# Performance work log

Hardware: AMD Instinct MI355X
Metric: run time of the kernel (lower is better)

## Reference

```python
import jax, jax.numpy as jnp
import numpy as np


def setup_inputs() -> dict:
    key = jax.random.key(0)
    k1, k2 = jax.random.split(key)
    x = jax.random.normal(k1, (16, 128, 64, 64), dtype=jnp.float32)
    # weight layout: [out_channels, in_channels, kh, kw], kernel must be 3 for the
    # original Python-loop bounds to match the allocated output size
    weight = jax.random.normal(k2, (256, 128, 3, 3), dtype=jnp.float32) * 0.05
    return {"x": x, "weight": weight}


def reference(x, weight):
    # Stride-1 conv2d with symmetric zero padding=1 (forward ignores bias/stride/
    # dilation/groups in the original module).
    pad = 1
    out = jax.lax.conv_general_dilated(
        x, weight,
        window_strides=(1, 1),
        padding=[(pad, pad), (pad, pad)],
        dimension_numbers=("NCHW", "OIHW", "NCHW"),
    )
    return out
```

## Files before the change

kernel.cpp:

```cpp
#include <hip/hip_runtime.h>
#include <hip/hip_bf16.h>
#include <stdint.h>

typedef short bf16x8 __attribute__((ext_vector_type(8)));
typedef float f32x16 __attribute__((ext_vector_type(16)));

#define N_IMG 16
#define C_IN  128
#define H_IMG 64
#define W_IMG 64
#define K_OUT 256

#define XB_BYTES (16ull*66*66*128*2)
#define WB_BYTES (36ull*8*2*64*16)
#define WS_NEED  (XB_BYTES + WB_BYTES)

#define LDSX_BYTES (6*66*256)

__device__ __forceinline__ void gload16(void* lds, const void* g) {
    __builtin_amdgcn_global_load_lds(
        (const __attribute__((address_space(1))) void*)g,
        (__attribute__((address_space(3))) void*)lds, 16, 0, 0);
}

__device__ __forceinline__ uint32_t pack2(float a, float b) {
    __hip_bfloat16 ha = __float2bfloat16(a), hb = __float2bfloat16(b);
    return (uint32_t)*(uint16_t*)&ha | ((uint32_t)*(uint16_t*)&hb << 16);
}

__global__ __launch_bounds__(256)
void transform_fused_kernel(const float* __restrict__ x, const float* __restrict__ w,
                            __hip_bfloat16* __restrict__ xb, __hip_bfloat16* __restrict__ wb) {
    __shared__ __align__(16) uint32_t xs[64 * 64];
    __shared__ float lw[1152];
    const int b = blockIdx.x;
    const int t = threadIdx.x;

    if (b < 1056) {
        const int yt = b % 66;
        const int n  = b / 66;
        const bool interior = (yt >= 1 && yt <= 64);

        if (interior) {
            const float4* src = (const float4*)(x + (size_t)n * 524288 + (size_t)(yt - 1) * 64);
            #pragma unroll
            for (int it = 0; it < 4; ++it) {
                const int x4 = t & 15;
                const int j  = (t >> 4) + it * 16;
                float4 va = src[(2 * j) * 1024 + x4];
                float4 vb = src[(2 * j + 1) * 1024 + x4];
                const float* pa = (const float*)&va;
                const float* pb = (const float*)&vb;
                #pragma unroll
                for (int i = 0; i < 4; ++i) {
                    int row = x4 * 4 + i;
                    xs[row * 64 + (j ^ (((row >> 2) & 3) << 2))] = pack2(pa[i], pb[i]);
                }
            }
        }
        __syncthreads();

        uint4* dst = (uint4*)((char*)xb + (size_t)(n * 66 + yt) * 66 * 256);
        #pragma unroll
        for (int it = 0; it < 5; ++it) {
            int ch = t + it * 256;
            if (ch < 1056) {
                int xt = ch >> 4, u = ch & 15;
                uint4 val = make_uint4(0u, 0u, 0u, 0u);
                if (interior && xt >= 1 && xt <= 64) {
                    int row = xt - 1;
                    val = *(const uint4*)&xs[row * 64 + 4 * (u ^ ((row >> 2) & 3))];
                }
                dst[ch] = val;
            }
        }
    } else {
        const int kg = b - 1056;
        for (int e = t; e < 1152; e += 256) lw[e] = w[kg * 1152 + e];
        __syncthreads();
        const int basek = (kg >> 5) * 1024 + (kg & 31) * 8;
        #pragma unroll
        for (int tap = 0; tap < 9; ++tap) {
            if (t < 128) {
                int c = t;
                int idx = (tap * 4 + (c >> 5)) * 8192 + basek
                        + ((c >> 4) & 1) * 512 + ((c >> 3) & 1) * 256 + (c & 7);
                wb[idx] = __float2bfloat16(lw[c * 9 + tap]);
            }
        }
    }
}

#define CHUNK(CC, AU, XBN)                                                                    \
  {                                                                                           \
    _Pragma("unroll") for (int f = 0; f < 4; ++f)                         \
      x1[f] = *(const bf16x8*)(lds + (xb0[f] ^ (((CC) << 6) | 32)));                          \
    __builtin_amdgcn_s_setprio(1);                                                            \
    _Pragma("unroll") for (int f = 0; f < 4; ++f) {                                           \
      acc[0][f] = __builtin_amdgcn_mfma_f32_32x32x16_bf16(AU[0][0], x0[f], acc[0][f], 0, 0, 0); \
      acc[1][f] = __builtin_amdgcn_mfma_f32_32x32x16_bf16(AU[1][0], x0[f], acc[1][f], 0, 0, 0); \
    }                                                                                         \
    __builtin_amdgcn_s_setprio(0);                                                            \
    _Pragma("unroll") for (int f = 0; f < 4; ++f)                       \
      x0[f] = *(const bf16x8*)(lds + ((XBN)[f] ^ ((((CC) + 1) & 3) << 6)));                   \
    __builtin_amdgcn_s_setprio(1);                                                            \
    _Pragma("unroll") for (int f = 0; f < 4; ++f) {                                           \
      acc[0][f] = __builtin_amdgcn_mfma_f32_32x32x16_bf16(AU[0][1], x1[f], acc[0][f], 0, 0, 0); \
      acc[1][f] = __builtin_amdgcn_mfma_f32_32x32x16_bf16(AU[1][1], x1[f], acc[1][f], 0, 0, 0); \
    }                                                                                         \
    __builtin_amdgcn_s_setprio(0);                                                            \
    { int jj = tap * 4 + (CC) + 2; if (jj >= 36) jj -= 36;                  \
      const char* wc = wgw + (size_t)jj * 16384;                                              \
      _Pragma("unroll") for (int kf = 0; kf < 2; ++kf)                                        \
        _Pragma("unroll") for (int ks = 0; ks < 2; ++ks)                                      \
          AU[kf][ks] = *(const bf16x8*)(wc + kf * 2048 + ks * 1024);                          \
    }                                                                                         \
  }

__global__ __launch_bounds__(512, 2)
void conv3x3_mfma_kernel(const char* __restrict__ xg,
                         const char* __restrict__ wg2,
                         float* __restrict__ out) {
    __shared__ uint4 smem[LDSX_BYTES / 16];
    char* lds = (char*)smem;

    const int t    = threadIdx.x;
    const int b    = blockIdx.x;
    const int q    = b & 15;
    const int n    = b >> 4;
    const int lane = t & 63;
    const int wv   = t >> 6;
    const int lm   = lane & 31;
    const int hi   = lane >> 5;
    const int kb   = (wv >> 1) * 64;
    const int mb   = (wv & 1) * 128;
    const int hi4  = hi * 16;

    int rc0[4];
    #pragma unroll
    for (int f = 0; f < 4; ++f) {
        int m = mb + f * 32 + lm;
        rc0[f] = (m >> 6) * 66 + (m & 63);
    }

    const char* xsrc = xg + (size_t)(n * 66 + q * 4) * 66 * 256;
    for (int ch = t; ch < 6336; ch += 512) {
        int L = ch * 16;
        gload16(lds + L, xsrc + (L ^ (((L >> 8) & 7) << 4)));
    }

    const char* wgw = wg2 + (wv >> 1) * 4096 + lane * 16;
    bf16x8 aA[2][2], aB[2][2];
    #pragma unroll
    for (int kf = 0; kf < 2; ++kf)
        #pragma unroll
        for (int ks = 0; ks < 2; ++ks) {
            aA[kf][ks] = *(const bf16x8*)(wgw + kf * 2048 + ks * 1024);
            aB[kf][ks] = *(const bf16x8*)(wgw + 16384 + kf * 2048 + ks * 1024);
        }

    asm volatile("s_waitcnt vmcnt(0)" ::: "memory");
    __syncthreads();

    f32x16 acc[2][4];
    #pragma unroll
    for (int i = 0; i < 2; ++i)
        #pragma unroll
        for (int j = 0; j < 4; ++j)
            acc[i][j] = (f32x16)(0.f);

    int xb0[4], xbN[4];
    #pragma unroll
    for (int f = 0; f < 4; ++f) {
        int rc = rc0[f];
        xbN[f] = rc * 256 + (hi4 ^ ((rc & 7) << 4));
    }

    bf16x8 x0[4], x1[4];
    #pragma unroll
    for (int f = 0; f < 4; ++f)
        x0[f] = *(const bf16x8*)(lds + xbN[f]);

    for (int tap = 0; tap < 9; ++tap) {
        #pragma unroll
        for (int f = 0; f < 4; ++f) xb0[f] = xbN[f];
        {
            int tn = (tap < 8) ? tap + 1 : 8;
            int rn = (tn >= 6) ? 2 : (tn >= 3 ? 1 : 0);
            int rs = rn * 66 + (tn - rn * 3);
            #pragma unroll
            for (int f = 0; f < 4; ++f) {
                int rc = rc0[f] + rs;
                xbN[f] = rc * 256 + (hi4 ^ ((rc & 7) << 4));
            }
        }
        CHUNK(0, aA, xb0)
        CHUNK(1, aB, xb0)
        CHUNK(2, aA, xb0)
        CHUNK(3, aB, xbN)
    }

    const int y0 = q * 4;
    #pragma unroll
    for (int kf = 0; kf < 2; ++kf) {
        const int kbase2 = kb + kf * 32 + 4 * hi;
        #pragma unroll
        for (int f = 0; f < 4; ++f) {
            int m  = mb + f * 32 + lm;
            int yy = m >> 6;
            int xx = m & 63;
            float* op = out + (((size_t)(n * 256 + kbase2) * 64) + y0 + yy) * 64 + xx;
            #pragma unroll
            for (int reg = 0; reg < 16; ++reg) {
                int koff = (reg & 3) + 8 * (reg >> 2);
                op[(size_t)koff * 4096] = acc[kf][f][reg];
            }
        }
    }
}

__global__ __launch_bounds__(256, 3)
void conv3x3_f32_kernel(const float* __restrict__ x,
                        const float* __restrict__ w,
                        float* __restrict__ out) {
    __shared__ float xs[16][3][72];
    __shared__ float ws[16][9][64];

    const int t  = threadIdx.x;
    const int kt = blockIdx.x & 3;
    const int y  = (blockIdx.x >> 2) & 63;
    const int n  = blockIdx.x >> 8;

    const int k2   = t >> 3;
    const int xg   = t & 7;
    const int kloc = k2 * 2;
    const int x0   = xg * 8;

    float acc0[8] = {0.f,0.f,0.f,0.f,0.f,0.f,0.f,0.f};
    float acc1[8] = {0.f,0.f,0.f,0.f,0.f,0.f,0.f,0.f};

    const int k0 = kt * 64;

    for (int c0 = 0; c0 < C_IN; c0 += 16) {
        for (int idx = t; idx < 16 * 3 * 66; idx += 256) {
            int col = idx % 66;
            int rc  = idx / 66;
            int r   = rc % 3;
            int c   = rc / 3;
            int gx  = col - 1;
            int gy  = y - 1 + r;
            float v = 0.f;
            if ((unsigned)gx < (unsigned)W_IMG && (unsigned)gy < (unsigned)H_IMG)
                v = x[(((n * C_IN) + c0 + c) * H_IMG + gy) * W_IMG + gx];
            xs[c][r][col] = v;
        }
        for (int idx = t; idx < 64 * 16 * 9; idx += 256) {
            int tap = idx % 9;
            int ck  = idx / 9;
            int c   = ck % 16;
            int k   = ck / 16;
            ws[c][tap][k] = w[((k0 + k) * C_IN + c0 + c) * 9 + tap];
        }
        __syncthreads();

        #pragma unroll 2
        for (int c = 0; c < 16; ++c) {
            #pragma unroll
            for (int r = 0; r < 3; ++r) {
                float xr[10];
                #pragma unroll
                for (int i = 0; i < 10; ++i) xr[i] = xs[c][r][x0 + i];
                #pragma unroll
                for (int s = 0; s < 3; ++s) {
                    float w0 = ws[c][r * 3 + s][kloc];
                    float w1 = ws[c][r * 3 + s][kloc + 1];
                    #pragma unroll
                    for (int i = 0; i < 8; ++i) {
                        acc0[i] = fmaf(w0, xr[i + s], acc0[i]);
                        acc1[i] = fmaf(w1, xr[i + s], acc1[i]);
                    }
                }
            }
        }
        __syncthreads();
    }

    float* o0 = &out[(((n * K_OUT) + k0 + kloc) * H_IMG + y) * W_IMG + x0];
    float* o1 = o0 + H_IMG * W_IMG;
    #pragma unroll
    for (int i = 0; i < 8; ++i) o0[i] = acc0[i];
    #pragma unroll
    for (int i = 0; i < 8; ++i) o1[i] = acc1[i];
}

extern "C" void kernel_launch(void* const* d_in, const int* in_sizes, int n_in,
                              void* d_out, int out_size, void* d_ws, size_t ws_size,
                              hipStream_t stream) {
    const float* x = (const float*)d_in[0];
    const float* w = (const float*)d_in[1];
    float* out = (float*)d_out;
    (void)in_sizes; (void)n_in; (void)out_size;

    if (ws_size >= WS_NEED) {
        __hip_bfloat16* xb = (__hip_bfloat16*)d_ws;
        __hip_bfloat16* wb = (__hip_bfloat16*)((char*)d_ws + XB_BYTES);
        transform_fused_kernel<<<1056 + 256, 256, 0, stream>>>(x, w, xb, wb);
        conv3x3_mfma_kernel<<<256, 512, 0, stream>>>((const char*)xb, (const char*)wb, out);
    } else {
        conv3x3_f32_kernel<<<4096, 256, 0, stream>>>(x, w, out);
    }
}
```

Baseline: 127.3 us.

## Halve conv tile to two output rows, double grid, raise occupancy

The MFMA conv kernel now has each block compute 2 output rows instead of 4, so the grid grows from 256 to 512 blocks and the LDS input tile shrinks to 4 padded rows. Waves are remapped so each of 8 waves covers 64 output channels by 64 pixels, with fewer accumulators, and launch bounds ask for 4 blocks per CU. The software pipeline that prefetched the next chunk's LDS fragments across iterations is replaced by simpler per-chunk loads with double-buffered weights. This aims to fill all CUs and hide latency through occupancy, at the cost of more halo-row reloads per output and less explicit overlap of LDS reads with MFMA.

```diff
diff --git a/kernel.cpp b/kernel.cpp
--- a/kernel.cpp
+++ b/kernel.cpp
@@ -15,7 +15,7 @@
 #define WB_BYTES (36ull*8*2*64*16)
 #define WS_NEED  (XB_BYTES + WB_BYTES)
 
-#define LDSX_BYTES (6*66*256)
+#define LDSX_BYTES (4*66*256)
 
 __device__ __forceinline__ void gload16(void* lds, const void* g) {
     __builtin_amdgcn_global_load_lds(
@@ -91,33 +91,31 @@
     }
 }
 
-#define CHUNK(CC, AU, XBN)                                                                    \
+#define DO_CHUNK(J, AUSE, ALOAD, RS66)                                                        \
   {                                                                                           \
-    _Pragma("unroll") for (int f = 0; f < 4; ++f)                         \
-      x1[f] = *(const bf16x8*)(lds + (xb0[f] ^ (((CC) << 6) | 32)));                          \
-    __builtin_amdgcn_s_setprio(1);                                                            \
-    _Pragma("unroll") for (int f = 0; f < 4; ++f) {                                           \
-      acc[0][f] = __builtin_amdgcn_mfma_f32_32x32x16_bf16(AU[0][0], x0[f], acc[0][f], 0, 0, 0); \
-      acc[1][f] = __builtin_amdgcn_mfma_f32_32x32x16_bf16(AU[1][0], x0[f], acc[1][f], 0, 0, 0); \
-    }                                                                                         \
-    __builtin_amdgcn_s_setprio(0);                                                            \
-    _Pragma("unroll") for (int f = 0; f < 4; ++f)                       \
-      x0[f] = *(const bf16x8*)(lds + ((XBN)[f] ^ ((((CC) + 1) & 3) << 6)));                   \
-    __builtin_amdgcn_s_setprio(1);                                                            \
-    _Pragma("unroll") for (int f = 0; f < 4; ++f) {                                           \
-      acc[0][f] = __builtin_amdgcn_mfma_f32_32x32x16_bf16(AU[0][1], x1[f], acc[0][f], 0, 0, 0); \
-      acc[1][f] = __builtin_amdgcn_mfma_f32_32x32x16_bf16(AU[1][1], x1[f], acc[1][f], 0, 0, 0); \
-    }                                                                                         \
-    __builtin_amdgcn_s_setprio(0);                                                            \
-    { int jj = tap * 4 + (CC) + 2; if (jj >= 36) jj -= 36;                  \
-      const char* wc = wgw + (size_t)jj * 16384;                                              \
+    int jn = (J) + 1; if (jn >= 36) jn = 0;                                                   \
+    const char* wc = wgw + (size_t)jn * 16384;                                                \
+    _Pragma("unroll") for (int kf = 0; kf < 2; ++kf)                                          \
+      _Pragma("unroll") for (int ks = 0; ks < 2; ++ks)                                        \
+        ALOAD[kf][ks] = *(const bf16x8*)(wc + kf * 2048 + ks * 1024);                         \
+    const int cc_ = (J) & 3;                                                                  \
+    _Pragma("unroll") for (int ks = 0; ks < 2; ++ks) {                                        \
+      bf16x8 xv[2];                                                                           \
+      _Pragma("unroll") for (int f = 0; f < 2; ++f) {                                         \
+        int rc  = rc0[f] + (RS66);                                                            \
+        int off = cc_ * 64 + ks * 32 + hi4;                                                   \
+        xv[f] = *(const bf16x8*)(lds + rc * 256 + (off ^ ((rc & 7) << 4)));                   \
+      }                                                                                       \
+      __builtin_amdgcn_s_setprio(1);                                                          \
       _Pragma("unroll") for (int kf = 0; kf < 2; ++kf)                                        \
-        _Pragma("unroll") for (int ks = 0; ks < 2; ++ks)                                      \
-          AU[kf][ks] = *(const bf16x8*)(wc + kf * 2048 + ks * 1024);                          \
+        _Pragma("unroll") for (int f = 0; f < 2; ++f)                                         \
+          acc[kf][f] = __builtin_amdgcn_mfma_f32_32x32x16_bf16(AUSE[kf][ks], xv[f],           \
+                                                               acc[kf][f], 0, 0, 0);         \
+      __builtin_amdgcn_s_setprio(0);                                                          \
     }                                                                                         \
   }
 
-__global__ __launch_bounds__(512, 2)
+__global__ __launch_bounds__(512, 4)
 void conv3x3_mfma_kernel(const char* __restrict__ xg,
                          const char* __restrict__ wg2,
                          float* __restrict__ out) {
@@ -126,86 +124,63 @@
 
     const int t    = threadIdx.x;
     const int b    = blockIdx.x;
-    const int q    = b & 15;
-    const int n    = b >> 4;
+    const int yp   = b & 31;
+    const int n    = b >> 5;
     const int lane = t & 63;
     const int wv   = t >> 6;
     const int lm   = lane & 31;
     const int hi   = lane >> 5;
-    const int kb   = (wv >> 1) * 64;
-    const int mb   = (wv & 1) * 128;
+    const int kb   = (wv & 3) * 64;
+    const int mb   = (wv >> 2) * 64;
     const int hi4  = hi * 16;
 
-    int rc0[4];
-    #pragma unroll
-    for (int f = 0; f < 4; ++f) {
+    int rc0[2];
+    #pragma unroll
+    for (int f = 0; f < 2; ++f) {
         int m = mb + f * 32 + lm;
         rc0[f] = (m >> 6) * 66 + (m & 63);
     }
 
-    const char* xsrc = xg + (size_t)(n * 66 + q * 4) * 66 * 256;
-    for (int ch = t; ch < 6336; ch += 512) {
+    const char* xsrc = xg + (size_t)(n * 66 + yp * 2) * 66 * 256;
+    for (int ch = t; ch < LDSX_BYTES / 16; ch += 512) {
         int L = ch * 16;
         gload16(lds + L, xsrc + (L ^ (((L >> 8) & 7) << 4)));
     }
 
-    const char* wgw = wg2 + (wv >> 1) * 4096 + lane * 16;
+    const char* wgw = wg2 + (kb >> 5) * 2048 + lane * 16;
     bf16x8 aA[2][2], aB[2][2];
     #pragma unroll
     for (int kf = 0; kf < 2; ++kf)
         #pragma unroll
-        for (int ks = 0; ks < 2; ++ks) {
+        for (int ks = 0; ks < 2; ++ks)
             aA[kf][ks] = *(const bf16x8*)(wgw + kf * 2048 + ks * 1024);
-            aB[kf][ks] = *(const bf16x8*)(wgw + 16384 + kf * 2048 + ks * 1024);
-        }
 
     asm volatile("s_waitcnt vmcnt(0)" ::: "memory");
     __syncthreads();
 
-    f32x16 acc[2][4];
+    f32x16 acc[2][2];
     #pragma unroll
     for (int i = 0; i < 2; ++i)
         #pragma unroll
-        for (int j = 0; j < 4; ++j)
+        for (int j = 0; j < 2; ++j)
             acc[i][j] = (f32x16)(0.f);
 
-    int xb0[4], xbN[4];
-    #pragma unroll
-    for (int f = 0; f < 4; ++f) {
-        int rc = rc0[f];
-        xbN[f] = rc * 256 + (hi4 ^ ((rc & 7) << 4));
-    }
-
-    bf16x8 x0[4], x1[4];
-    #pragma unroll
-    for (int f = 0; f < 4; ++f)
-        x0[f] = *(const bf16x8*)(lds + xbN[f]);
-
     for (int tap = 0; tap < 9; ++tap) {
-        #pragma unroll
-        for (int f = 0; f < 4; ++f) xb0[f] = xbN[f];
-        {
-            int tn = (tap < 8) ? tap + 1 : 8;
-            int rn = (tn >= 6) ? 2 : (tn >= 3 ? 1 : 0);
-            int rs = rn * 66 + (tn - rn * 3);
-            #pragma unroll
-            for (int f = 0; f < 4; ++f) {
-                int rc = rc0[f] + rs;
-                xbN[f] = rc * 256 + (hi4 ^ ((rc & 7) << 4));
-            }
-        }
-        CHUNK(0, aA, xb0)
-        CHUNK(1, aB, xb0)
-        CHUNK(2, aA, xb0)
-        CHUNK(3, aB, xbN)
-    }
-
-    const int y0 = q * 4;
+        const int r    = (tap >= 6) ? 2 : (tap >= 3 ? 1 : 0);
+        const int rs66 = r * 66 + (tap - r * 3);
+        const int j0   = tap * 4;
+        DO_CHUNK(j0 + 0, aA, aB, rs66)
+        DO_CHUNK(j0 + 1, aB, aA, rs66)
+        DO_CHUNK(j0 + 2, aA, aB, rs66)
+        DO_CHUNK(j0 + 3, aB, aA, rs66)
+    }
+
+    const int y0 = yp * 2;
     #pragma unroll
     for (int kf = 0; kf < 2; ++kf) {
         const int kbase2 = kb + kf * 32 + 4 * hi;
         #pragma unroll
-        for (int f = 0; f < 4; ++f) {
+        for (int f = 0; f < 2; ++f) {
             int m  = mb + f * 32 + lm;
             int yy = m >> 6;
             int xx = m & 63;
@@ -305,7 +280,7 @@
         __hip_bfloat16* xb = (__hip_bfloat16*)d_ws;
         __hip_bfloat16* wb = (__hip_bfloat16*)((char*)d_ws + XB_BYTES);
         transform_fused_kernel<<<1056 + 256, 256, 0, stream>>>(x, w, xb, wb);
-        conv3x3_mfma_kernel<<<256, 512, 0, stream>>>((const char*)xb, (const char*)wb, out);
+        conv3x3_mfma_kernel<<<512, 512, 0, stream>>>((const char*)xb, (const char*)wb, out);
     } else {
         conv3x3_f32_kernel<<<4096, 256, 0, stream>>>(x, w, out);
     }
```

Measured after the change: 132.8 us. +4.3%, slower.
